# Optimization experiments

Hardware: AMD Instinct MI355X
Metric: run time of the kernel (lower is better)

## Reference

```python
import jax, jax.numpy as jnp
import numpy as np

IN_DIM, H_DIM, Y_DIM, ROLLOUT = 1024, 2048, 1024, 512


def setup_inputs() -> dict:
    key = jax.random.key(0)
    ks = jax.random.split(key, 4)
    return {
        "x": jax.random.normal(ks[0], (1, ROLLOUT, IN_DIM), dtype=jnp.float32),
        "h": jnp.zeros((H_DIM,), dtype=jnp.float32),
        "Wc": jax.random.normal(ks[1], (IN_DIM + H_DIM, H_DIM), dtype=jnp.float32) * 0.01,
        "Wu": jax.random.normal(ks[2], (IN_DIM + H_DIM, H_DIM), dtype=jnp.float32) * 0.01,
        "bc": jnp.zeros((H_DIM,), dtype=jnp.float32),
        "bu": jnp.zeros((H_DIM,), dtype=jnp.float32),
        "Wh_y": jax.random.normal(ks[3], (H_DIM, Y_DIM), dtype=jnp.float32) * 0.01,
        "by": jnp.zeros((Y_DIM,), dtype=jnp.float32),
    }


def reference(x, h, Wc, Wu, bc, bu, Wh_y, by):
    # x: [1, T, in_dim]; h: [h_dim]. Strict sequential GRU-style cell via scan.
    def step(h_prev, xt):
        xc = jnp.concatenate([xt, h_prev])           # [in+h]
        Lu = jax.nn.sigmoid(xc @ Wu + bu)            # update gate
        c_tilda = jnp.tanh(xc @ Wc + bc)             # candidate
        h_new = Lu * c_tilda + (1.0 - Lu) * h_prev
        y = h_new @ Wh_y + by
        return h_new, y

    h_final, ys = jax.lax.scan(step, h, x[0])        # ys: [T, y_dim]
    return ys, h_final
```

## Files before the change

### kernel.cpp

```cpp
#include <hip/hip_runtime.h>
#include <hip/hip_bf16.h>
#include <math.h>

#define T_STEPS 512
#define IN_DIM  1024
#define H_DIM   2048
#define Y_DIM   1024

#define NBLK2 128
#define BT2   512
#define NWORD (H_DIM / 2)

static __device__ __forceinline__ unsigned f2bf(float f) {
    unsigned u = __float_as_uint(f);
    return ((u + 0x7FFFu + ((u >> 16) & 1u)) >> 16) & 0xFFFFu;
}
static __device__ __forceinline__ float bflo(unsigned p) { return __uint_as_float(p << 16); }
static __device__ __forceinline__ float bfhi(unsigned p) { return __uint_as_float(p & 0xFFFF0000u); }

#define TM 64
#define TN 128
#define TK 16

__global__ __launch_bounds__(256) void gemm_bias(
    const float* __restrict__ A, const float* __restrict__ B,
    const float* __restrict__ bias, float* __restrict__ C,
    int M, int N, int K, int lda, int ldb, int ldc)
{
    __shared__ float As[TK][TM + 4];
    __shared__ float Bs[TK][TN + 4];

    const int n0 = blockIdx.x * TN;
    const int m0 = blockIdx.y * TM;
    const int tid = threadIdx.x;
    const int tx = tid & 15;
    const int ty = tid >> 4;

    float acc[4][8] = {};

    for (int k0 = 0; k0 < K; k0 += TK) {
        {
            int mm = tid & 63, kq = tid >> 6;
            float4 a = *(const float4*)&A[(m0 + mm) * lda + k0 + 4 * kq];
            As[4 * kq + 0][mm] = a.x;
            As[4 * kq + 1][mm] = a.y;
            As[4 * kq + 2][mm] = a.z;
            As[4 * kq + 3][mm] = a.w;
        }
        #pragma unroll
        for (int l = tid; l < 512; l += 256) {
            int kk = l >> 5, jj = (l & 31) * 4;
            *(float4*)&Bs[kk][jj] = *(const float4*)&B[(k0 + kk) * ldb + n0 + jj];
        }
        __syncthreads();
        #pragma unroll
        for (int kk = 0; kk < TK; ++kk) {
            float4 a  = *(const float4*)&As[kk][ty * 4];
            float4 b0 = *(const float4*)&Bs[kk][tx * 8];
            float4 b1 = *(const float4*)&Bs[kk][tx * 8 + 4];
            const float av[4] = {a.x, a.y, a.z, a.w};
            const float bv[8] = {b0.x, b0.y, b0.z, b0.w, b1.x, b1.y, b1.z, b1.w};
            #pragma unroll
            for (int r = 0; r < 4; ++r)
                #pragma unroll
                for (int c = 0; c < 8; ++c)
                    acc[r][c] = fmaf(av[r], bv[c], acc[r][c]);
        }
        __syncthreads();
    }

    float4 bv0 = *(const float4*)&bias[n0 + tx * 8];
    float4 bv1 = *(const float4*)&bias[n0 + tx * 8 + 4];
    const float bb[8] = {bv0.x, bv0.y, bv0.z, bv0.w, bv1.x, bv1.y, bv1.z, bv1.w};
    #pragma unroll
    for (int r = 0; r < 4; ++r) {
        float4 o0, o1;
        o0.x = acc[r][0] + bb[0]; o0.y = acc[r][1] + bb[1];
        o0.z = acc[r][2] + bb[2]; o0.w = acc[r][3] + bb[3];
        o1.x = acc[r][4] + bb[4]; o1.y = acc[r][5] + bb[5];
        o1.z = acc[r][6] + bb[6]; o1.w = acc[r][7] + bb[7];
        float* cp = &C[(m0 + ty * 4 + r) * ldc + n0 + tx * 8];
        *(float4*)cp = o0;
        *(float4*)(cp + 4) = o1;
    }
}

__global__ __launch_bounds__(BT2) void gru_seq(
    const float* __restrict__ Wu_h,
    const float* __restrict__ Wc_h,
    const float* __restrict__ XU,
    const float* __restrict__ XC,
    const float* __restrict__ h0,
    unsigned long long* __restrict__ Hp,
    float* __restrict__ H)
{
    __shared__ float hbuf[2][10496];

    const int tid  = threadIdx.x;
    const int w    = tid >> 6;
    const int lane = tid & 63;
    const int jb   = blockIdx.x * 16;
    const int j0   = jb + 2 * w;

    unsigned wru0[16], wru1[16], wrc0[16], wrc1[16];
    #pragma unroll
    for (int q = 0; q < 8; ++q) {
        int e = 4 * (q * 64 + lane);
        const float* u = Wu_h + (size_t)e * H_DIM + j0;
        const float* c = Wc_h + (size_t)e * H_DIM + j0;
        wru0[2*q]   = f2bf(u[0])              | (f2bf(u[(size_t)H_DIM])     << 16);
        wru0[2*q+1] = f2bf(u[2*(size_t)H_DIM]) | (f2bf(u[3*(size_t)H_DIM])  << 16);
        wru1[2*q]   = f2bf(u[1])              | (f2bf(u[(size_t)H_DIM+1])   << 16);
        wru1[2*q+1] = f2bf(u[2*(size_t)H_DIM+1]) | (f2bf(u[3*(size_t)H_DIM+1]) << 16);
        wrc0[2*q]   = f2bf(c[0])              | (f2bf(c[(size_t)H_DIM])     << 16);
        wrc0[2*q+1] = f2bf(c[2*(size_t)H_DIM]) | (f2bf(c[3*(size_t)H_DIM])  << 16);
        wrc1[2*q]   = f2bf(c[1])              | (f2bf(c[(size_t)H_DIM+1])   << 16);
        wrc1[2*q+1] = f2bf(c[2*(size_t)H_DIM+1]) | (f2bf(c[3*(size_t)H_DIM+1]) << 16);
    }

    float hc0 = h0[j0], hc1 = h0[j0 + 1];
    const int myword = blockIdx.x * 8 + w;

    for (int t = 0; t < T_STEPS; ++t) {
        float2 xu = make_float2(0.f, 0.f), xc = make_float2(0.f, 0.f);
        if (lane == 0) {
            xu = *(const float2*)(XU + (size_t)t * H_DIM + j0);
            xc = *(const float2*)(XC + (size_t)t * H_DIM + j0);
        }

        float* hb = hbuf[t & 1];

        if (t == 0) {
            *(float4*)&hb[4 * tid] = *(const float4*)&h0[4 * tid];
        } else {
            const unsigned long long* src = Hp + (size_t)(t - 1) * NWORD;
            unsigned long long p0 =
                __hip_atomic_load(src + 2 * tid,     __ATOMIC_RELAXED, __HIP_MEMORY_SCOPE_AGENT);
            unsigned long long p1 =
                __hip_atomic_load(src + 2 * tid + 1, __ATOMIC_RELAXED, __HIP_MEMORY_SCOPE_AGENT);
            const unsigned tag = (unsigned)t;
            int s0 = (unsigned)(p0 >> 32) != tag;
            int s1 = (unsigned)(p1 >> 32) != tag;
            while (__any(s0 | s1)) {
                __builtin_amdgcn_s_sleep(1);
                if (s0) {
                    p0 = __hip_atomic_load(src + 2 * tid, __ATOMIC_RELAXED, __HIP_MEMORY_SCOPE_AGENT);
                    s0 = (unsigned)(p0 >> 32) != tag;
                }
                if (s1) {
                    p1 = __hip_atomic_load(src + 2 * tid + 1, __ATOMIC_RELAXED, __HIP_MEMORY_SCOPE_AGENT);
                    s1 = (unsigned)(p1 >> 32) != tag;
                }
            }
            float4 hv;
            hv.x = bflo((unsigned)p0);
            hv.y = bfhi((unsigned)p0);
            hv.z = bflo((unsigned)p1);
            hv.w = bfhi((unsigned)p1);
            *(float4*)&hb[4 * tid] = hv;
        }
        __syncthreads();

        float au0 = 0.f, au1 = 0.f, ac0 = 0.f, ac1 = 0.f;
        #pragma unroll
        for (int q = 0; q < 8; ++q) {
            float4 h4 = *(const float4*)&hb[4 * (q * 64 + lane)];
            unsigned a, b;
            a = wru0[2*q]; b = wru0[2*q+1];
            au0 = fmaf(h4.x, bflo(a), au0); au0 = fmaf(h4.y, bfhi(a), au0);
            au0 = fmaf(h4.z, bflo(b), au0); au0 = fmaf(h4.w, bfhi(b), au0);
            a = wru1[2*q]; b = wru1[2*q+1];
            au1 = fmaf(h4.x, bflo(a), au1); au1 = fmaf(h4.y, bfhi(a), au1);
            au1 = fmaf(h4.z, bflo(b), au1); au1 = fmaf(h4.w, bfhi(b), au1);
            a = wrc0[2*q]; b = wrc0[2*q+1];
            ac0 = fmaf(h4.x, bflo(a), ac0); ac0 = fmaf(h4.y, bfhi(a), ac0);
            ac0 = fmaf(h4.z, bflo(b), ac0); ac0 = fmaf(h4.w, bfhi(b), ac0);
            a = wrc1[2*q]; b = wrc1[2*q+1];
            ac1 = fmaf(h4.x, bflo(a), ac1); ac1 = fmaf(h4.y, bfhi(a), ac1);
            ac1 = fmaf(h4.z, bflo(b), ac1); ac1 = fmaf(h4.w, bfhi(b), ac1);
        }
        #pragma unroll
        for (int off = 32; off; off >>= 1) {
            au0 += __shfl_down(au0, off);
            au1 += __shfl_down(au1, off);
            ac0 += __shfl_down(ac0, off);
            ac1 += __shfl_down(ac1, off);
        }

        if (lane == 0) {
            float pu0 = au0 + xu.x, pu1 = au1 + xu.y;
            float pc0 = ac0 + xc.x, pc1 = ac1 + xc.y;
            float ug0 = 1.f / (1.f + __expf(-pu0));
            float ug1 = 1.f / (1.f + __expf(-pu1));
            float e0 = __expf(-2.f * fabsf(pc0));
            float e1 = __expf(-2.f * fabsf(pc1));
            float cg0 = copysignf((1.f - e0) / (1.f + e0), pc0);
            float cg1 = copysignf((1.f - e1) / (1.f + e1), pc1);
            float hn0 = ug0 * cg0 + (1.f - ug0) * hc0;
            float hn1 = ug1 * cg1 + (1.f - ug1) * hc1;
            hc0 = hn0; hc1 = hn1;

            unsigned lo = f2bf(hn0) | (f2bf(hn1) << 16);
            __hip_atomic_store(Hp + (size_t)t * NWORD + myword,
                               ((unsigned long long)(unsigned)(t + 1) << 32) | lo,
                               __ATOMIC_RELAXED, __HIP_MEMORY_SCOPE_AGENT);
            *(float2*)(H + (size_t)t * H_DIM + j0) = make_float2(hn0, hn1);
        }
    }
}

extern "C" void kernel_launch(void* const* d_in, const int* in_sizes, int n_in,
                              void* d_out, int out_size, void* d_ws, size_t ws_size,
                              hipStream_t stream)
{
    const float* x   = (const float*)d_in[0];
    const float* h0  = (const float*)d_in[1];
    const float* Wc  = (const float*)d_in[2];
    const float* Wu  = (const float*)d_in[3];
    const float* bc  = (const float*)d_in[4];
    const float* bu  = (const float*)d_in[5];
    const float* Why = (const float*)d_in[6];
    const float* by  = (const float*)d_in[7];
    float* out = (float*)d_out;

    float* ws = (float*)d_ws;
    float* XU = ws;
    float* XC = ws + (T_STEPS * H_DIM);
    float* H  = ws + 2 * (T_STEPS * H_DIM);
    unsigned long long* Hp =
        (unsigned long long*)(ws + 3 * (T_STEPS * H_DIM));

    gemm_bias<<<dim3(H_DIM / TN, T_STEPS / TM), 256, 0, stream>>>(
        x, Wu, bu, XU, T_STEPS, H_DIM, IN_DIM, IN_DIM, H_DIM, H_DIM);
    gemm_bias<<<dim3(H_DIM / TN, T_STEPS / TM), 256, 0, stream>>>(
        x, Wc, bc, XC, T_STEPS, H_DIM, IN_DIM, IN_DIM, H_DIM, H_DIM);

    gru_seq<<<NBLK2, BT2, 0, stream>>>(
        Wu + IN_DIM * H_DIM, Wc + IN_DIM * H_DIM, XU, XC, h0, Hp, H);

    gemm_bias<<<dim3(Y_DIM / TN, T_STEPS / TM), 256, 0, stream>>>(
        H, Why, by, out, T_STEPS, Y_DIM, H_DIM, H_DIM, Y_DIM, Y_DIM);

    hipMemcpyAsync(out + T_STEPS * Y_DIM, H + (T_STEPS - 1) * H_DIM,
                   H_DIM * sizeof(float), hipMemcpyDeviceToDevice, stream);
}
```

Baseline: 2.378 ms.

## Poll hidden state with one wavefront using exponential backoff and prefetch gate inputs

The spin-wait on the previous step's packed hidden state now runs in wavefront 0 alone. Each lane loads 16 words, and the wave retries with exponential s_sleep backoff, where before all 8 waves polled with a fixed sleep. The precomputed input projections for the next step are loaded one iteration ahead to hide their latency. This cuts polling traffic on the flag words, but the backoff can add latency after a value arrives, and a single wave now does all of the LDS fill.

```diff
diff --git a/kernel.cpp b/kernel.cpp
--- a/kernel.cpp
+++ b/kernel.cpp
@@ -17,6 +17,17 @@
 }
 static __device__ __forceinline__ float bflo(unsigned p) { return __uint_as_float(p << 16); }
 static __device__ __forceinline__ float bfhi(unsigned p) { return __uint_as_float(p & 0xFFFF0000u); }
+
+static __device__ __forceinline__ void sleep_bk(int r) {
+    switch (r) {
+        case 0: break;
+        case 1: __builtin_amdgcn_s_sleep(1); break;
+        case 2: __builtin_amdgcn_s_sleep(2); break;
+        case 3: __builtin_amdgcn_s_sleep(4); break;
+        case 4: __builtin_amdgcn_s_sleep(8); break;
+        default: __builtin_amdgcn_s_sleep(16); break;
+    }
+}
 
 #define TM 64
 #define TN 128
@@ -108,56 +119,68 @@
         int e = 4 * (q * 64 + lane);
         const float* u = Wu_h + (size_t)e * H_DIM + j0;
         const float* c = Wc_h + (size_t)e * H_DIM + j0;
-        wru0[2*q]   = f2bf(u[0])              | (f2bf(u[(size_t)H_DIM])     << 16);
-        wru0[2*q+1] = f2bf(u[2*(size_t)H_DIM]) | (f2bf(u[3*(size_t)H_DIM])  << 16);
-        wru1[2*q]   = f2bf(u[1])              | (f2bf(u[(size_t)H_DIM+1])   << 16);
+        wru0[2*q]   = f2bf(u[0])               | (f2bf(u[(size_t)H_DIM])      << 16);
+        wru0[2*q+1] = f2bf(u[2*(size_t)H_DIM]) | (f2bf(u[3*(size_t)H_DIM])    << 16);
+        wru1[2*q]   = f2bf(u[1])               | (f2bf(u[(size_t)H_DIM+1])    << 16);
         wru1[2*q+1] = f2bf(u[2*(size_t)H_DIM+1]) | (f2bf(u[3*(size_t)H_DIM+1]) << 16);
-        wrc0[2*q]   = f2bf(c[0])              | (f2bf(c[(size_t)H_DIM])     << 16);
-        wrc0[2*q+1] = f2bf(c[2*(size_t)H_DIM]) | (f2bf(c[3*(size_t)H_DIM])  << 16);
-        wrc1[2*q]   = f2bf(c[1])              | (f2bf(c[(size_t)H_DIM+1])   << 16);
+        wrc0[2*q]   = f2bf(c[0])               | (f2bf(c[(size_t)H_DIM])      << 16);
+        wrc0[2*q+1] = f2bf(c[2*(size_t)H_DIM]) | (f2bf(c[3*(size_t)H_DIM])    << 16);
+        wrc1[2*q]   = f2bf(c[1])               | (f2bf(c[(size_t)H_DIM+1])    << 16);
         wrc1[2*q+1] = f2bf(c[2*(size_t)H_DIM+1]) | (f2bf(c[3*(size_t)H_DIM+1]) << 16);
     }
 
     float hc0 = h0[j0], hc1 = h0[j0 + 1];
     const int myword = blockIdx.x * 8 + w;
 
+    float2 xu_cur = make_float2(0.f, 0.f), xc_cur = make_float2(0.f, 0.f);
+    if (lane == 0) {
+        xu_cur = *(const float2*)(XU + j0);
+        xc_cur = *(const float2*)(XC + j0);
+    }
+
     for (int t = 0; t < T_STEPS; ++t) {
-        float2 xu = make_float2(0.f, 0.f), xc = make_float2(0.f, 0.f);
-        if (lane == 0) {
-            xu = *(const float2*)(XU + (size_t)t * H_DIM + j0);
-            xc = *(const float2*)(XC + (size_t)t * H_DIM + j0);
+        float2 xu_nxt = make_float2(0.f, 0.f), xc_nxt = make_float2(0.f, 0.f);
+        if (lane == 0 && t + 1 < T_STEPS) {
+            xu_nxt = *(const float2*)(XU + (size_t)(t + 1) * H_DIM + j0);
+            xc_nxt = *(const float2*)(XC + (size_t)(t + 1) * H_DIM + j0);
         }
 
         float* hb = hbuf[t & 1];
 
         if (t == 0) {
             *(float4*)&hb[4 * tid] = *(const float4*)&h0[4 * tid];
-        } else {
+        } else if (w == 0) {
             const unsigned long long* src = Hp + (size_t)(t - 1) * NWORD;
-            unsigned long long p0 =
-                __hip_atomic_load(src + 2 * tid,     __ATOMIC_RELAXED, __HIP_MEMORY_SCOPE_AGENT);
-            unsigned long long p1 =
-                __hip_atomic_load(src + 2 * tid + 1, __ATOMIC_RELAXED, __HIP_MEMORY_SCOPE_AGENT);
             const unsigned tag = (unsigned)t;
-            int s0 = (unsigned)(p0 >> 32) != tag;
-            int s1 = (unsigned)(p1 >> 32) != tag;
-            while (__any(s0 | s1)) {
-                __builtin_amdgcn_s_sleep(1);
-                if (s0) {
-                    p0 = __hip_atomic_load(src + 2 * tid, __ATOMIC_RELAXED, __HIP_MEMORY_SCOPE_AGENT);
-                    s0 = (unsigned)(p0 >> 32) != tag;
-                }
-                if (s1) {
-                    p1 = __hip_atomic_load(src + 2 * tid + 1, __ATOMIC_RELAXED, __HIP_MEMORY_SCOPE_AGENT);
-                    s1 = (unsigned)(p1 >> 32) != tag;
-                }
+            unsigned long long v[16];
+            #pragma unroll
+            for (int i = 0; i < 16; ++i)
+                v[i] = __hip_atomic_load(src + i * 64 + lane,
+                                         __ATOMIC_RELAXED, __HIP_MEMORY_SCOPE_AGENT);
+            unsigned mask = 0;
+            #pragma unroll
+            for (int i = 0; i < 16; ++i)
+                mask |= ((unsigned)(v[i] >> 32) != tag) ? (1u << i) : 0u;
+
+            int rnd = 0;
+            while (__any(mask != 0u)) {
+                sleep_bk(rnd);
+                if (rnd < 5) ++rnd;
+                #pragma unroll
+                for (int i = 0; i < 16; ++i)
+                    if (mask & (1u << i))
+                        v[i] = __hip_atomic_load(src + i * 64 + lane,
+                                                 __ATOMIC_RELAXED, __HIP_MEMORY_SCOPE_AGENT);
+                #pragma unroll
+                for (int i = 0; i < 16; ++i)
+                    if ((mask & (1u << i)) && (unsigned)(v[i] >> 32) == tag)
+                        mask &= ~(1u << i);
             }
-            float4 hv;
-            hv.x = bflo((unsigned)p0);
-            hv.y = bfhi((unsigned)p0);
-            hv.z = bflo((unsigned)p1);
-            hv.w = bfhi((unsigned)p1);
-            *(float4*)&hb[4 * tid] = hv;
+            #pragma unroll
+            for (int i = 0; i < 16; ++i) {
+                unsigned lo = (unsigned)v[i];
+                *(float2*)&hb[2 * (i * 64 + lane)] = make_float2(bflo(lo), bfhi(lo));
+            }
         }
         __syncthreads();
 
@@ -188,8 +211,8 @@
         }
 
         if (lane == 0) {
-            float pu0 = au0 + xu.x, pu1 = au1 + xu.y;
-            float pc0 = ac0 + xc.x, pc1 = ac1 + xc.y;
+            float pu0 = au0 + xu_cur.x, pu1 = au1 + xu_cur.y;
+            float pc0 = ac0 + xc_cur.x, pc1 = ac1 + xc_cur.y;
             float ug0 = 1.f / (1.f + __expf(-pu0));
             float ug1 = 1.f / (1.f + __expf(-pu1));
             float e0 = __expf(-2.f * fabsf(pc0));
@@ -206,6 +229,7 @@
                                __ATOMIC_RELAXED, __HIP_MEMORY_SCOPE_AGENT);
             *(float2*)(H + (size_t)t * H_DIM + j0) = make_float2(hn0, hn1);
         }
+        xu_cur = xu_nxt; xc_cur = xc_nxt;
     }
 }
 
@@ -241,6 +265,6 @@
     gemm_bias<<<dim3(Y_DIM / TN, T_STEPS / TM), 256, 0, stream>>>(
         H, Why, by, out, T_STEPS, Y_DIM, H_DIM, H_DIM, Y_DIM, Y_DIM);
 
-    hipMemcpyAsync(out + T_STEPS * Y_DIM, H + (T_STEPS - 1) * H_DIM,
-                   H_DIM * sizeof(float), hipMemcpyDeviceToDevice, stream);
-}
+    (void)hipMemcpyAsync(out + T_STEPS * Y_DIM, H + (T_STEPS - 1) * H_DIM,
+                         H_DIM * sizeof(float), hipMemcpyDeviceToDevice, stream);
+}
```

After: 2.566 ms. +7.9%, slower.
